# Kernel tuning notes

Measured on AMD Instinct MI355X. Metric: run time of the kernel, lower is better.

Reference implementation:

```python
import jax, jax.numpy as jnp
import numpy as np

B = 65536
NUM_INPUTS = 256
NUM_HIDDEN = 256


def setup_inputs() -> dict:
    key = jax.random.key(0)
    ks = jax.random.split(key, 11)
    f32 = jnp.float32
    return {
        "x": jax.random.normal(ks[0], (B, NUM_INPUTS), dtype=f32),
        "h_t_1": jax.random.normal(ks[1], (B, NUM_HIDDEN), dtype=f32),
        "Wz": jax.random.normal(ks[2], (NUM_INPUTS, NUM_HIDDEN), dtype=f32),
        "Uz": jax.random.normal(ks[3], (NUM_HIDDEN, NUM_HIDDEN), dtype=f32),
        "bz": jax.random.normal(ks[4], (NUM_HIDDEN,), dtype=f32),
        "Wr": jax.random.normal(ks[5], (NUM_INPUTS, NUM_HIDDEN), dtype=f32),
        "Ur": jax.random.normal(ks[6], (NUM_HIDDEN, NUM_HIDDEN), dtype=f32),
        "br": jax.random.normal(ks[7], (NUM_HIDDEN,), dtype=f32),
        "Wh": jax.random.normal(ks[8], (NUM_INPUTS, NUM_HIDDEN), dtype=f32),
        "Uh": jax.random.normal(ks[9], (NUM_HIDDEN, NUM_HIDDEN), dtype=f32),
        "bh": jax.random.normal(ks[10], (NUM_HIDDEN,), dtype=f32),
    }


def reference(x, h_t_1, Wz, Uz, bz, Wr, Ur, br, Wh, Uh, bh):
    # update gate z = sigmoid(x@Wz + h@Uz + bz)
    z = jax.nn.sigmoid(x @ Wz + h_t_1 @ Uz + bz)
    # reset gate r = sigmoid(x@Wr + h@Ur + br)
    r = jax.nn.sigmoid(x @ Wr + h_t_1 @ Ur + br)
    # candidate: tanh(x@Wh + (r*h)@Uh + bh)
    h_hat = jnp.tanh(x @ Wh + (r * h_t_1) @ Uh + bh)
    h_t = z * h_t_1 + (1.0 - z) * h_hat
    return (h_t, h_t)
```

## Files before the change

kernel.cpp:

```cpp
#include <hip/hip_runtime.h>
#include <hip/hip_fp16.h>


#define NHID 256
#define B_ROWS 65536
#define MT 64
#define RT 4
#define CPW 2
#define GATE_STRIDE (16 * 16 * 64 * 8)

typedef _Float16 half8 __attribute__((ext_vector_type(8)));
typedef _Float16 half4_t __attribute__((ext_vector_type(4)));
typedef _Float16 half2_t __attribute__((ext_vector_type(2)));
typedef float floatx4 __attribute__((ext_vector_type(4)));

__device__ __forceinline__ int lidx(int m, int c) {
    return m * 256 + ((((c >> 3) ^ (m & 7)) << 3)) + (c & 7);
}

__device__ __forceinline__ void barrier_lgkm() {
    __builtin_amdgcn_sched_barrier(0);
    asm volatile("s_waitcnt lgkmcnt(0)" ::: "memory");
    __builtin_amdgcn_s_barrier();
    __builtin_amdgcn_sched_barrier(0);
}

__global__ __launch_bounds__(256) void pack_weights_kernel(
    const float* __restrict__ Wz, const float* __restrict__ Uz,
    const float* __restrict__ Wr, const float* __restrict__ Ur,
    const float* __restrict__ Wh, const float* __restrict__ Uh,
    _Float16* __restrict__ packed)
{
    int tid = blockIdx.x * blockDim.x + threadIdx.x;
    int lane = tid & 63;
    int s    = (tid >> 6) & 15;
    int ct   = (tid >> 10) & 15;
    int g    = tid >> 14;
    const float* W = (g == 0) ? Wz : (g == 1) ? Wr : Wh;
    const float* U = (g == 0) ? Uz : (g == 1) ? Ur : Uh;
    int n  = ct * 16 + (lane & 15);
    int k0 = s * 32 + (lane >> 4) * 8;
    half8 v;
#pragma unroll
    for (int j = 0; j < 8; ++j) {
        int k = k0 + j;
        float f = (k < 256) ? W[k * 256 + n] : U[(k - 256) * 256 + n];
        v[j] = (_Float16)f;
    }
    *reinterpret_cast<half8*>(packed + (size_t)tid * 8) = v;
}

#define WFRAG(base, ct, s) \
    (*reinterpret_cast<const half8*>((base) + (size_t)((((ct) * 16 + (s)) * 64 + lane) * 8)))

__global__ __launch_bounds__(512, 2) void gru_main_kernel(
    const float* __restrict__ x, const float* __restrict__ h,
    const _Float16* __restrict__ wpack,
    const float* __restrict__ bz, const float* __restrict__ br,
    const float* __restrict__ bh,
    float* __restrict__ out)
{
    __shared__ __align__(16) _Float16 lsm[MT * 256 * 2];
    _Float16* lx = lsm;
    _Float16* lh = lsm + MT * 256;

    const int tid  = threadIdx.x;
    const int lane = tid & 63;
    const int wave = tid >> 6;
    const int row0 = blockIdx.x * MT;
    const int m_lo = lane & 15;
    const int quad = lane >> 4;
    const int mx   = m_lo & 7;
    const int ct0  = wave * CPW;

    const _Float16* wz = wpack;
    const _Float16* wr = wpack + GATE_STRIDE;
    const _Float16* wh = wpack + 2 * GATE_STRIDE;

    half8 wzb[2][CPW], wrb[2][CPW];
    wzb[0][0] = WFRAG(wz, ct0 + 0, 0);
    wzb[0][1] = WFRAG(wz, ct0 + 1, 0);
    wrb[0][0] = WFRAG(wr, ct0 + 0, 0);
    wrb[0][1] = WFRAG(wr, ct0 + 1, 0);

    {
        const float4* xv = reinterpret_cast<const float4*>(x + (size_t)row0 * NHID);
        const float4* hv = reinterpret_cast<const float4*>(h + (size_t)row0 * NHID);
#pragma unroll
        for (int it = 0; it < (MT * 64) / 512; ++it) {
            int i = it * 512 + tid;
            int m = i >> 6;
            int c = (i & 63) * 4;
            float4 a = xv[i];
            float4 b = hv[i];
            half4_t va = { (_Float16)a.x, (_Float16)a.y, (_Float16)a.z, (_Float16)a.w };
            half4_t vb = { (_Float16)b.x, (_Float16)b.y, (_Float16)b.z, (_Float16)b.w };
            *reinterpret_cast<half4_t*>(&lx[lidx(m, c)]) = va;
            *reinterpret_cast<half4_t*>(&lh[lidx(m, c)]) = vb;
        }
    }
    barrier_lgkm();

    half2_t zpk[CPW][RT][4];

    floatx4 accz[CPW][RT];
    floatx4 accr[CPW][RT];
#pragma unroll
    for (int c = 0; c < CPW; ++c)
#pragma unroll
        for (int rt = 0; rt < RT; ++rt) {
            accz[c][rt] = (floatx4){0.f, 0.f, 0.f, 0.f};
            accr[c][rt] = (floatx4){0.f, 0.f, 0.f, 0.f};
        }

#pragma unroll
    for (int s = 0; s < 16; ++s) {
        const int cur = s & 1, nxt = cur ^ 1;
        if (s < 15) {
            wzb[nxt][0] = WFRAG(wz, ct0 + 0, s + 1);
            wzb[nxt][1] = WFRAG(wz, ct0 + 1, s + 1);
            wrb[nxt][0] = WFRAG(wr, ct0 + 0, s + 1);
            wrb[nxt][1] = WFRAG(wr, ct0 + 1, s + 1);
        }
        const _Float16* asrc = (s < 8) ? lx : lh;
        const int kcx = (((s & 7) * 4 + quad) ^ mx) << 3;
        half8 af[RT];
#pragma unroll
        for (int rt = 0; rt < RT; ++rt)
            af[rt] = *reinterpret_cast<const half8*>(&asrc[(rt * 16 + m_lo) * 256 + kcx]);
        __builtin_amdgcn_s_setprio(1);
#pragma unroll
        for (int c = 0; c < CPW; ++c)
#pragma unroll
            for (int rt = 0; rt < RT; ++rt) {
                accz[c][rt] = __builtin_amdgcn_mfma_f32_16x16x32_f16(af[rt], wzb[cur][c], accz[c][rt], 0, 0, 0);
                accr[c][rt] = __builtin_amdgcn_mfma_f32_16x16x32_f16(af[rt], wrb[cur][c], accr[c][rt], 0, 0, 0);
            }
        __builtin_amdgcn_s_setprio(0);
    }

    half8 whb[2][CPW];
    whb[0][0] = WFRAG(wh, ct0 + 0, 0);
    whb[0][1] = WFRAG(wh, ct0 + 1, 0);
    float bzv[CPW], brv[CPW], bhv[CPW];
#pragma unroll
    for (int c = 0; c < CPW; ++c) {
        const int col = (ct0 + c) * 16 + m_lo;
        bzv[c] = bz[col];
        brv[c] = br[col];
        bhv[c] = bh[col];
    }

    barrier_lgkm();

#pragma unroll
    for (int c = 0; c < CPW; ++c) {
        const int col = (ct0 + c) * 16 + m_lo;
#pragma unroll
        for (int rt = 0; rt < RT; ++rt) {
#pragma unroll
            for (int e = 0; e < 4; ++e) {
                const int row = rt * 16 + quad * 4 + e;
                float sz = accz[c][rt][e] + bzv[c];
                float sr = accr[c][rt][e] + brv[c];
                float zv = 1.f / (1.f + __expf(-sz));
                float rv = 1.f / (1.f + __expf(-sr));
                const int li = lidx(row, col);
                float hval = (float)lh[li];
                lh[li] = (_Float16)(rv * hval);
                zpk[c][rt][e] = half2_t{ (_Float16)(zv * hval), (_Float16)(1.f - zv) };
            }
        }
    }

    barrier_lgkm();

    floatx4 acch[CPW][RT];
#pragma unroll
    for (int c = 0; c < CPW; ++c)
#pragma unroll
        for (int rt = 0; rt < RT; ++rt)
            acch[c][rt] = (floatx4){0.f, 0.f, 0.f, 0.f};

#pragma unroll
    for (int s = 0; s < 16; ++s) {
        const int cur = s & 1, nxt = cur ^ 1;
        if (s < 15) {
            whb[nxt][0] = WFRAG(wh, ct0 + 0, s + 1);
            whb[nxt][1] = WFRAG(wh, ct0 + 1, s + 1);
        }
        const _Float16* asrc = (s < 8) ? lx : lh;
        const int kcx = (((s & 7) * 4 + quad) ^ mx) << 3;
        half8 af[RT];
#pragma unroll
        for (int rt = 0; rt < RT; ++rt)
            af[rt] = *reinterpret_cast<const half8*>(&asrc[(rt * 16 + m_lo) * 256 + kcx]);
        __builtin_amdgcn_s_setprio(1);
#pragma unroll
        for (int c = 0; c < CPW; ++c)
#pragma unroll
            for (int rt = 0; rt < RT; ++rt)
                acch[c][rt] = __builtin_amdgcn_mfma_f32_16x16x32_f16(af[rt], whb[cur][c], acch[c][rt], 0, 0, 0);
        __builtin_amdgcn_s_setprio(0);
    }

    const size_t OUT2 = (size_t)B_ROWS * NHID;
#pragma unroll
    for (int c = 0; c < CPW; ++c) {
        const int col = (ct0 + c) * 16 + m_lo;
#pragma unroll
        for (int rt = 0; rt < RT; ++rt) {
#pragma unroll
            for (int e = 0; e < 4; ++e) {
                const int row = rt * 16 + quad * 4 + e;
                float sh = acch[c][rt][e] + bhv[c];
                float e2 = __expf(2.f * sh);
                float hh = 1.f - 2.f / (e2 + 1.f);
                float zh  = (float)zpk[c][rt][e][0];
                float omz = (float)zpk[c][rt][e][1];
                float ht  = zh + omz * hh;
                size_t idx = (size_t)(row0 + row) * NHID + col;
                __builtin_nontemporal_store(ht, &out[idx]);
                __builtin_nontemporal_store(ht, &out[OUT2 + idx]);
            }
        }
    }
}

extern "C" void kernel_launch(void* const* d_in, const int* in_sizes, int n_in,
                              void* d_out, int out_size, void* d_ws, size_t ws_size,
                              hipStream_t stream) {
    (void)in_sizes; (void)n_in; (void)out_size; (void)ws_size;
    const float* x  = (const float*)d_in[0];
    const float* h  = (const float*)d_in[1];
    const float* Wz = (const float*)d_in[2];
    const float* Uz = (const float*)d_in[3];
    const float* bz = (const float*)d_in[4];
    const float* Wr = (const float*)d_in[5];
    const float* Ur = (const float*)d_in[6];
    const float* br = (const float*)d_in[7];
    const float* Wh = (const float*)d_in[8];
    const float* Uh = (const float*)d_in[9];
    const float* bh = (const float*)d_in[10];
    float* out = (float*)d_out;
    _Float16* wpack = (_Float16*)d_ws;

    pack_weights_kernel<<<192, 256, 0, stream>>>(Wz, Uz, Wr, Ur, Wh, Uh, wpack);
    gru_main_kernel<<<B_ROWS / MT, 512, 0, stream>>>(x, h, wpack, bz, br, bh, out);
}
```

Before: 312.1 us.

## Shrink row tile to 32 with 4 waves each covering 4 column tiles

Blocks now cover 32 rows with 256 threads (4 waves), and each wave owns 4 column tiles instead of 2. The weight-fragment double buffer is restructured to prefetch half a wave's column tiles at a time, alternating between column pairs within each K step. This doubles the block count and cuts LDS per block, which should raise occupancy and spread work more finely. In exchange, each weight fragment is reused across fewer rows (RT=2), so per-row weight traffic from L2 goes up.

```diff
diff --git a/kernel.cpp b/kernel.cpp
--- a/kernel.cpp
+++ b/kernel.cpp
@@ -4,9 +4,9 @@
 
 #define NHID 256
 #define B_ROWS 65536
-#define MT 64
-#define RT 4
-#define CPW 2
+#define MT 32
+#define RT 2
+#define CPW 4
 #define GATE_STRIDE (16 * 16 * 64 * 8)
 
 typedef _Float16 half8 __attribute__((ext_vector_type(8)));
@@ -53,7 +53,7 @@
 #define WFRAG(base, ct, s) \
     (*reinterpret_cast<const half8*>((base) + (size_t)((((ct) * 16 + (s)) * 64 + lane) * 8)))
 
-__global__ __launch_bounds__(512, 2) void gru_main_kernel(
+__global__ __launch_bounds__(256, 4) void gru_main_kernel(
     const float* __restrict__ x, const float* __restrict__ h,
     const _Float16* __restrict__ wpack,
     const float* __restrict__ bz, const float* __restrict__ br,
@@ -77,7 +77,7 @@
     const _Float16* wr = wpack + GATE_STRIDE;
     const _Float16* wh = wpack + 2 * GATE_STRIDE;
 
-    half8 wzb[2][CPW], wrb[2][CPW];
+    half8 wzb[2][2], wrb[2][2];
     wzb[0][0] = WFRAG(wz, ct0 + 0, 0);
     wzb[0][1] = WFRAG(wz, ct0 + 1, 0);
     wrb[0][0] = WFRAG(wr, ct0 + 0, 0);
@@ -87,8 +87,8 @@
         const float4* xv = reinterpret_cast<const float4*>(x + (size_t)row0 * NHID);
         const float4* hv = reinterpret_cast<const float4*>(h + (size_t)row0 * NHID);
 #pragma unroll
-        for (int it = 0; it < (MT * 64) / 512; ++it) {
-            int i = it * 512 + tid;
+        for (int it = 0; it < (MT * 64) / 256; ++it) {
+            int i = it * 256 + tid;
             int m = i >> 6;
             int c = (i & 63) * 4;
             float4 a = xv[i];
@@ -115,31 +115,38 @@
 
 #pragma unroll
     for (int s = 0; s < 16; ++s) {
-        const int cur = s & 1, nxt = cur ^ 1;
-        if (s < 15) {
-            wzb[nxt][0] = WFRAG(wz, ct0 + 0, s + 1);
-            wzb[nxt][1] = WFRAG(wz, ct0 + 1, s + 1);
-            wrb[nxt][0] = WFRAG(wr, ct0 + 0, s + 1);
-            wrb[nxt][1] = WFRAG(wr, ct0 + 1, s + 1);
-        }
         const _Float16* asrc = (s < 8) ? lx : lh;
         const int kcx = (((s & 7) * 4 + quad) ^ mx) << 3;
         half8 af[RT];
 #pragma unroll
         for (int rt = 0; rt < RT; ++rt)
             af[rt] = *reinterpret_cast<const half8*>(&asrc[(rt * 16 + m_lo) * 256 + kcx]);
-        __builtin_amdgcn_s_setprio(1);
-#pragma unroll
-        for (int c = 0; c < CPW; ++c)
-#pragma unroll
-            for (int rt = 0; rt < RT; ++rt) {
-                accz[c][rt] = __builtin_amdgcn_mfma_f32_16x16x32_f16(af[rt], wzb[cur][c], accz[c][rt], 0, 0, 0);
-                accr[c][rt] = __builtin_amdgcn_mfma_f32_16x16x32_f16(af[rt], wrb[cur][c], accr[c][rt], 0, 0, 0);
-            }
-        __builtin_amdgcn_s_setprio(0);
-    }
-
-    half8 whb[2][CPW];
+#pragma unroll
+        for (int p = 0; p < 2; ++p) {
+            const int u = s * 2 + p;
+            if (u < 31) {
+                const int ns = (p == 1) ? s + 1 : s;
+                const int nc = ct0 + (p ^ 1) * 2;
+                wzb[p ^ 1][0] = WFRAG(wz, nc + 0, ns);
+                wzb[p ^ 1][1] = WFRAG(wz, nc + 1, ns);
+                wrb[p ^ 1][0] = WFRAG(wr, nc + 0, ns);
+                wrb[p ^ 1][1] = WFRAG(wr, nc + 1, ns);
+            }
+            __builtin_amdgcn_s_setprio(1);
+#pragma unroll
+            for (int q = 0; q < 2; ++q) {
+                const int c = p * 2 + q;
+#pragma unroll
+                for (int rt = 0; rt < RT; ++rt) {
+                    accz[c][rt] = __builtin_amdgcn_mfma_f32_16x16x32_f16(af[rt], wzb[p][q], accz[c][rt], 0, 0, 0);
+                    accr[c][rt] = __builtin_amdgcn_mfma_f32_16x16x32_f16(af[rt], wrb[p][q], accr[c][rt], 0, 0, 0);
+                }
+            }
+            __builtin_amdgcn_s_setprio(0);
+        }
+    }
+
+    half8 whb[2][2];
     whb[0][0] = WFRAG(wh, ct0 + 0, 0);
     whb[0][1] = WFRAG(wh, ct0 + 1, 0);
     float bzv[CPW], brv[CPW], bhv[CPW];
@@ -184,24 +191,31 @@
 
 #pragma unroll
     for (int s = 0; s < 16; ++s) {
-        const int cur = s & 1, nxt = cur ^ 1;
-        if (s < 15) {
-            whb[nxt][0] = WFRAG(wh, ct0 + 0, s + 1);
-            whb[nxt][1] = WFRAG(wh, ct0 + 1, s + 1);
-        }
         const _Float16* asrc = (s < 8) ? lx : lh;
         const int kcx = (((s & 7) * 4 + quad) ^ mx) << 3;
         half8 af[RT];
 #pragma unroll
         for (int rt = 0; rt < RT; ++rt)
             af[rt] = *reinterpret_cast<const half8*>(&asrc[(rt * 16 + m_lo) * 256 + kcx]);
-        __builtin_amdgcn_s_setprio(1);
-#pragma unroll
-        for (int c = 0; c < CPW; ++c)
-#pragma unroll
-            for (int rt = 0; rt < RT; ++rt)
-                acch[c][rt] = __builtin_amdgcn_mfma_f32_16x16x32_f16(af[rt], whb[cur][c], acch[c][rt], 0, 0, 0);
-        __builtin_amdgcn_s_setprio(0);
+#pragma unroll
+        for (int p = 0; p < 2; ++p) {
+            const int u = s * 2 + p;
+            if (u < 31) {
+                const int ns = (p == 1) ? s + 1 : s;
+                const int nc = ct0 + (p ^ 1) * 2;
+                whb[p ^ 1][0] = WFRAG(wh, nc + 0, ns);
+                whb[p ^ 1][1] = WFRAG(wh, nc + 1, ns);
+            }
+            __builtin_amdgcn_s_setprio(1);
+#pragma unroll
+            for (int q = 0; q < 2; ++q) {
+                const int c = p * 2 + q;
+#pragma unroll
+                for (int rt = 0; rt < RT; ++rt)
+                    acch[c][rt] = __builtin_amdgcn_mfma_f32_16x16x32_f16(af[rt], whb[p][q], acch[c][rt], 0, 0, 0);
+            }
+            __builtin_amdgcn_s_setprio(0);
+        }
     }
 
     const size_t OUT2 = (size_t)B_ROWS * NHID;
@@ -246,5 +260,5 @@
     _Float16* wpack = (_Float16*)d_ws;
 
     pack_weights_kernel<<<192, 256, 0, stream>>>(Wz, Uz, Wr, Ur, Wh, Uh, wpack);
-    gru_main_kernel<<<B_ROWS / MT, 512, 0, stream>>>(x, h, wpack, bz, br, bh, out);
-}
+    gru_main_kernel<<<B_ROWS / MT, 256, 0, stream>>>(x, h, wpack, bz, br, bh, out);
+}
```

Measured after the change: 356.8 us. +14.3%, slower.
